# Kernel optimization log

Measured on AMD Instinct MI355X. Metric: run time of the kernel, lower is better.

Reference implementation:

```python
import jax, jax.numpy as jnp
import numpy as np

NUM_HEADS = 8


def setup_inputs() -> dict:
    key = jax.random.key(0)
    ks = jax.random.split(key, 7)
    B, D, N = 16, 512, 2048
    sc = 1.0 / np.sqrt(D)
    return {
        "X_Query": jax.random.normal(ks[0], (B, D, N), jnp.float32),
        "X_Key": jax.random.normal(ks[1], (B, D, N), jnp.float32),
        "X_Value": jax.random.normal(ks[2], (B, D, N), jnp.float32),
        "W_q": jax.random.normal(ks[3], (D, D), jnp.float32) * sc,
        "W_k": jax.random.normal(ks[4], (D, D), jnp.float32) * sc,
        "W_v": jax.random.normal(ks[5], (D, D), jnp.float32) * sc,
        "W_o": jax.random.normal(ks[6], (D, D), jnp.float32) * sc,
    }


def _proj(W, x):
    # Conv1d(D, D, kernel_size=1, bias=False) == channel matmul
    return jnp.einsum('oi,bin->bon', W, x)


def _split_heads(x, h):
    # torch: cat(x.chunk(h, dim=-1), dim=0) -> (h, B, D, N/h) stacked layout
    B, D, N = x.shape
    return x.reshape(B, D, h, N // h).transpose(2, 0, 1, 3)


def _mha(XQ, XK, XV, Wq, Wk, Wv, Wo):
    B, D, N = XQ.shape
    h = NUM_HEADS
    Nh = N // h
    q = _split_heads(_proj(Wq, XQ), h)  # (h, B, D, Nh)
    k = _split_heads(_proj(Wk, XK), h)
    v = _split_heads(_proj(Wv, XV), h)
    # scores over the CHANNEL axis: (h, B, D, D), scaled by sqrt(d_k)=sqrt(Nh)
    scores = jnp.einsum('hbdn,hben->hbde', q, k) / jnp.sqrt(jnp.asarray(Nh, q.dtype))
    p = jax.nn.softmax(scores, axis=-1)
    out = jnp.einsum('hbde,hben->hbdn', p, v)  # (h, B, D, Nh)
    # torch: cat(chunks, dim=0) inverse -> cat along dim=-1
    attn_heads = out.transpose(1, 2, 0, 3).reshape(B, D, N)
    return _proj(Wo, XQ - attn_heads)


def reference(X_Query, X_Key, X_Value, W_q, W_k, W_v, W_o):
    return _mha(X_Query, X_Key, X_Value, W_q, W_k, W_v, W_o)
```

## Files before the change

### kernel.cpp

```cpp
#include <hip/hip_runtime.h>
#include <hip/hip_bf16.h>

#define DD  512
#define NN  2048
#define BB  16
#define NHD 256

typedef unsigned short u16;
typedef __attribute__((ext_vector_type(4))) float f32x4;
typedef __attribute__((ext_vector_type(8))) short s16x8;
typedef __attribute__((ext_vector_type(4))) u16   u16x4;

static __device__ __forceinline__ u16 f2bf(float f) {
  __hip_bfloat16 h = __float2bfloat16(f);
  return *reinterpret_cast<u16*>(&h);
}
static __device__ __forceinline__ float bf2f(u16 u) {
  union { unsigned int i; float f; } v; v.i = ((unsigned int)u) << 16; return v.f;
}
static __device__ __forceinline__ f32x4 mfma_bf16(s16x8 a, s16x8 b, f32x4 c) {
  return __builtin_amdgcn_mfma_f32_16x16x32_bf16(a, b, c, 0, 0, 0);
}
static __device__ __forceinline__ void gload_lds16(const u16* g, u16* l) {
  __builtin_amdgcn_global_load_lds(
      (const __attribute__((address_space(1))) unsigned int*)g,
      (__attribute__((address_space(3))) unsigned int*)l, 16, 0, 0);
}
static __device__ __forceinline__ void barrier_raw() {
  __builtin_amdgcn_sched_barrier(0);
  __builtin_amdgcn_s_barrier();
  __builtin_amdgcn_sched_barrier(0);
}
#define WAITCNT(s) do { asm volatile("s_waitcnt " s ::: "memory"); \
                        __builtin_amdgcn_sched_barrier(0); } while (0)

__global__ __launch_bounds__(256) void k_cvt_w(const float* __restrict__ w0,
                                               const float* __restrict__ w1,
                                               const float* __restrict__ w2,
                                               const float* __restrict__ w3,
                                               u16* __restrict__ out) {
  const float* srcs[4] = {w0, w1, w2, w3};
  const float* s = srcs[blockIdx.y];
  u16* o = out + (size_t)blockIdx.y * (DD * DD);
  int idx = blockIdx.x * 256 + threadIdx.x;
  float4 v = *(const float4*)(s + (size_t)idx * 4);
  u16x4 u = {f2bf(v.x), f2bf(v.y), f2bf(v.z), f2bf(v.w)};
  *(u16x4*)(o + (size_t)idx * 4) = u;
}

__global__ __launch_bounds__(256) void k_transpose(const float* __restrict__ X,
                                                   u16* __restrict__ XT) {
  __shared__ float t[64][68];
  const int tid = threadIdx.x;
  const int n0 = blockIdx.x * 64, d0 = blockIdx.y * 64, b = blockIdx.z;
  const float* Xb = X + ((size_t)b * DD + d0) * NN + n0;
#pragma unroll
  for (int i = 0; i < 4; ++i) {
    int r = (tid >> 4) + i * 16;
    int c = (tid & 15) * 4;
    float4 v = *(const float4*)(Xb + (size_t)r * NN + c);
    t[r][c] = v.x; t[r][c + 1] = v.y; t[r][c + 2] = v.z; t[r][c + 3] = v.w;
  }
  __syncthreads();
  u16* Ob = XT + ((size_t)b * NN + n0) * DD + d0;
#pragma unroll
  for (int i = 0; i < 4; ++i) {
    int n = (tid >> 4) + i * 16;
    int d = (tid & 15) * 4;
    u16x4 u = {f2bf(t[d][n]), f2bf(t[d + 1][n]), f2bf(t[d + 2][n]), f2bf(t[d + 3][n])};
    *(u16x4*)(Ob + (size_t)n * DD + d) = u;
  }
}

#define GEMM_STAGE(Ag, lda, Bg, ldb, buf, kt)                                   \
  {                                                                             \
    _Pragma("unroll")                                                           \
    for (int j = 0; j < 4; ++j) {                                               \
      int s = j * 256 + w * 64 + lane;                                          \
      int row = s >> 3, u = s & 7;                                              \
      int col = ((u ^ (row & 7)) * 8);                                          \
      gload_lds16(Ag + (size_t)row * lda + (kt) * 64 + col, &Ab[buf][s * 8]);   \
      gload_lds16(Bg + (size_t)row * ldb + (kt) * 64 + col, &Bb[buf][s * 8]);   \
    }                                                                           \
  }

#define GEMM_COMPUTE(buf)                                                       \
  {                                                                             \
    _Pragma("unroll")                                                           \
    for (int ks = 0; ks < 2; ++ks) {                                            \
      s16x8 av[4], bv[4];                                                       \
      _Pragma("unroll")                                                         \
      for (int m = 0; m < 4; ++m) {                                             \
        int row = wm + m * 16 + r;                                              \
        av[m] = *(const s16x8*)&Ab[buf][row * 64 + (((ks * 4 + g) ^ (row & 7)) * 8)]; \
      }                                                                         \
      _Pragma("unroll")                                                         \
      for (int nf = 0; nf < 4; ++nf) {                                          \
        int row = wn + nf * 16 + r;                                             \
        bv[nf] = *(const s16x8*)&Bb[buf][row * 64 + (((ks * 4 + g) ^ (row & 7)) * 8)]; \
      }                                                                         \
      _Pragma("unroll")                                                         \
      for (int m = 0; m < 4; ++m)                                               \
        _Pragma("unroll")                                                       \
        for (int nf = 0; nf < 4; ++nf)                                          \
          acc[m][nf] = mfma_bf16(av[m], bv[nf], acc[m][nf]);                    \
    }                                                                           \
  }

#define GEMM_PREAMBLE                                                           \
  __shared__ __align__(16) u16 Ab[2][128 * 64];                                 \
  __shared__ __align__(16) u16 Bb[2][128 * 64];                                 \
  const int tid = threadIdx.x;                                                  \
  const int lane = tid & 63, w = tid >> 6;                                      \
  const int wm = (w >> 1) * 64, wn = (w & 1) * 64;                              \
  const int r = lane & 15, g = lane >> 4;                                       \
  f32x4 acc[4][4] = {};

#define GEMM_MAINLOOP(Ag, lda, Bg, ldb, nkt)                                    \
  GEMM_STAGE(Ag, lda, Bg, ldb, 0, 0);                                           \
  __syncthreads();                                                              \
  for (int kt = 0; kt < (nkt) - 1; ++kt) {                                      \
    GEMM_STAGE(Ag, lda, Bg, ldb, (kt & 1) ^ 1, kt + 1);                         \
    GEMM_COMPUTE(kt & 1);                                                       \
    __syncthreads();                                                            \
  }                                                                             \
  GEMM_COMPUTE(((nkt) - 1) & 1);

template <typename OUT_T>
__global__ __launch_bounds__(256) void k_gemm_nt(
    const u16* __restrict__ A, long long a_bs, int lda,
    const u16* __restrict__ B, long long b_bs, int ldb,
    OUT_T* __restrict__ C, long long c_bs, int ldc, int K) {
  GEMM_PREAMBLE
  const int m0 = blockIdx.x * 128, n0 = blockIdx.y * 128;
  const u16* Ag = A + (size_t)blockIdx.z * a_bs + (size_t)m0 * lda;
  const u16* Bg = B + (size_t)blockIdx.z * b_bs + (size_t)n0 * ldb;
  const int nkt = K >> 6;
  GEMM_MAINLOOP(Ag, lda, Bg, ldb, nkt);

  OUT_T* Cg = C + (size_t)blockIdx.z * c_bs;
#pragma unroll
  for (int m = 0; m < 4; ++m)
#pragma unroll
    for (int nf = 0; nf < 4; ++nf)
#pragma unroll
      for (int j = 0; j < 4; ++j) {
        int row = m0 + wm + m * 16 + g * 4 + j;
        int col = n0 + wn + nf * 16 + r;
        float v = acc[m][nf][j];
        if constexpr (sizeof(OUT_T) == 2) Cg[(size_t)row * ldc + col] = f2bf(v);
        else                              Cg[(size_t)row * ldc + col] = v;
      }
}

__global__ __launch_bounds__(512, 4) void k_attn_fused(
    const u16* __restrict__ Qdn, const u16* __restrict__ Kdn,
    const u16* __restrict__ VT,  const u16* __restrict__ XqT,
    u16* __restrict__ And) {
  __shared__ __align__(16) u16 L[37376];
  u16* Ks = L;
  u16* Vs = L + 16384;
  u16* Ps = L + 32768;

  const int tid = threadIdx.x;
  const int lane = tid & 63, w = tid >> 6;
  const int r = lane & 15, g = lane >> 4;
  const int dq = w >> 1, eh = w & 1;
  const int nq = w >> 1, dh = w & 1;
  const int bid = blockIdx.x;
  const int dt = bid >> 7, hb = bid & 127;
  const int h = hb & 7, b = hb >> 3;
  const int d0 = dt * 64, hn0 = h * NHD;

  const u16* Qg = Qdn + ((size_t)b * DD + d0) * NN + hn0;
  const u16* Kg = Kdn + ((size_t)b * DD) * NN + hn0;
  const u16* Vg = VT + ((size_t)b * NN + hn0) * DD;

  auto stage_k = [&](int idx) {
    const int e0 = (idx >> 1) * 64, c0 = (idx & 1) * 128;
    u16* dst = Ks + (idx & 1) * 8192;
#pragma unroll
    for (int j = 0; j < 2; ++j) {
      int s = j * 512 + tid;
      int row = s >> 4, u = s & 15;
      gload_lds16(Kg + (size_t)(e0 + row) * NN + c0 + ((u ^ (row & 7)) * 8), dst + s * 8);
    }
  };
  auto stage_v = [&](int t) {
    u16* dst = Vs + (t & 1) * 8192;
#pragma unroll
    for (int j = 0; j < 2; ++j) {
      int s = j * 512 + tid;
      int row = s >> 2, u = s & 3;
      gload_lds16(Vg + (size_t)row * DD + t * 32 + ((u ^ ((row >> 1) & 3)) * 8), dst + s * 8);
    }
  };

  stage_k(0);
#pragma unroll
  for (int j = 0; j < 4; ++j) {
    int s = j * 512 + tid;
    int row = s >> 5, u = s & 31;
    gload_lds16(Qg + (size_t)row * NN + ((u ^ (row & 7)) * 8), Vs + s * 8);
  }
  WAITCNT("vmcnt(0)");
  barrier_raw();
  s16x8 qf[8];
#pragma unroll
  for (int k2 = 0; k2 < 8; ++k2) {
    int row = dq * 16 + r;
    qf[k2] = *(const s16x8*)&Vs[row * 256 + (((k2 * 4 + g) ^ (row & 7)) * 8)];
  }
  WAITCNT("lgkmcnt(0)");
  barrier_raw();

  float psum[4] = {};
  f32x4 acc_o[4][2] = {};

  for (int et = 0; et < 8; ++et) {
    f32x4 acc_s[2] = {};
#pragma unroll
    for (int nsub = 0; nsub < 2; ++nsub) {
      const int idx = et * 2 + nsub;
      stage_v(idx);
      if (idx < 15) {
        stage_k(idx + 1);
        WAITCNT("vmcnt(4)");
      } else {
        WAITCNT("vmcnt(2)");
      }
      barrier_raw();
      const u16* kb = Ks + (idx & 1) * 8192;
#pragma unroll
      for (int kq = 0; kq < 4; ++kq) {
        s16x8 bv[2];
#pragma unroll
        for (int nf = 0; nf < 2; ++nf) {
          int rowe = eh * 32 + nf * 16 + r;
          bv[nf] = *(const s16x8*)&kb[rowe * 128 + (((kq * 4 + g) ^ (rowe & 7)) * 8)];
        }
        acc_s[0] = mfma_bf16(qf[nsub * 4 + kq], bv[0], acc_s[0]);
        acc_s[1] = mfma_bf16(qf[nsub * 4 + kq], bv[1], acc_s[1]);
      }
      WAITCNT("lgkmcnt(0)");
      barrier_raw();
    }
#pragma unroll
    for (int nf = 0; nf < 2; ++nf)
#pragma unroll
      for (int j = 0; j < 4; ++j) {
        int rowd = dq * 16 + g * 4 + j;
        int cole = eh * 32 + nf * 16 + r;
        float p = __expf(acc_s[nf][j] * 0.0625f);
        psum[j] += p;
        Ps[rowd * 72 + cole] = f2bf(p);
      }
    WAITCNT("lgkmcnt(0)");
    if (et < 7) WAITCNT("vmcnt(2)");
    else        WAITCNT("vmcnt(0)");
    barrier_raw();
#pragma unroll
    for (int vs = 0; vs < 2; ++vs) {
      s16x8 pb[2];
#pragma unroll
      for (int nf = 0; nf < 2; ++nf) {
        int rowd = dh * 32 + nf * 16 + r;
        pb[nf] = *(const s16x8*)&Ps[rowd * 72 + vs * 32 + g * 8];
      }
      const u16* vb = Vs + vs * 8192;
#pragma unroll
      for (int ms = 0; ms < 4; ++ms) {
        int rown = nq * 64 + ms * 16 + r;
        s16x8 av = *(const s16x8*)&vb[rown * 32 + ((g ^ ((rown >> 1) & 3)) * 8)];
        acc_o[ms][0] = mfma_bf16(av, pb[0], acc_o[ms][0]);
        acc_o[ms][1] = mfma_bf16(av, pb[1], acc_o[ms][1]);
      }
    }
    WAITCNT("lgkmcnt(0)");
    barrier_raw();
  }

  float* rs = (float*)L;
#pragma unroll
  for (int j = 0; j < 4; ++j) {
    float v = psum[j];
    v += __shfl_xor(v, 1);
    v += __shfl_xor(v, 2);
    v += __shfl_xor(v, 4);
    v += __shfl_xor(v, 8);
    if (r == 0) rs[w * 16 + g * 4 + j] = v;
  }
  __syncthreads();
  if (tid < 64) {
    int dqi = tid >> 4, i = tid & 15;
    rs[128 + tid] = 1.0f / (rs[(dqi * 2) * 16 + i] + rs[(dqi * 2 + 1) * 16 + i]);
  }
  __syncthreads();

  const u16* Xg = XqT + ((size_t)b * NN + hn0) * DD + d0;
  u16* Ag = And + ((size_t)b * NN + hn0) * DD + d0;
#pragma unroll
  for (int ms = 0; ms < 4; ++ms)
#pragma unroll
    for (int nf = 0; nf < 2; ++nf) {
      const int cold = dh * 32 + nf * 16 + r;
      const float inv = rs[128 + cold];
#pragma unroll
      for (int j = 0; j < 4; ++j) {
        const int npos = nq * 64 + ms * 16 + g * 4 + j;
        float o = acc_o[ms][nf][j] * inv;
        float xq = bf2f(Xg[(size_t)npos * DD + cold]);
        Ag[(size_t)npos * DD + cold] = f2bf(xq - o);
      }
    }
}

extern "C" void kernel_launch(void* const* d_in, const int* in_sizes, int n_in,
                              void* d_out, int out_size, void* d_ws, size_t ws_size,
                              hipStream_t stream) {
  const float* Xq = (const float*)d_in[0];
  const float* Xk = (const float*)d_in[1];
  const float* Xv = (const float*)d_in[2];
  const float* Wq = (const float*)d_in[3];
  const float* Wk = (const float*)d_in[4];
  const float* Wv = (const float*)d_in[5];
  const float* Wo = (const float*)d_in[6];
  float* out = (float*)d_out;

  char* ws = (char*)d_ws;
  const size_t MB = 1024 * 1024;
  u16* Wb  = (u16*)ws;
  u16* XqT = (u16*)(ws + 2 * MB);
  u16* Z2  = (u16*)(ws + 34 * MB);
  u16* And = Z2;
  u16* Qdn = (u16*)(ws + 66 * MB);
  u16* VTb = (u16*)d_out;
  u16* Kdn = (u16*)d_out + (size_t)BB * NN * DD;

  k_cvt_w<<<dim3(256, 4), 256, 0, stream>>>(Wq, Wk, Wv, Wo, Wb);

  k_transpose<<<dim3(NN / 64, DD / 64, BB), 256, 0, stream>>>(Xv, Z2);
  k_gemm_nt<u16><<<dim3(NN / 128, DD / 128, BB), 256, 0, stream>>>(
      Z2, (long long)NN * DD, DD,
      Wb + 2 * DD * DD, 0, DD,
      VTb, (long long)NN * DD, DD, DD);

  k_transpose<<<dim3(NN / 64, DD / 64, BB), 256, 0, stream>>>(Xq, XqT);
  k_gemm_nt<u16><<<dim3(DD / 128, NN / 128, BB), 256, 0, stream>>>(
      Wb, 0, DD,
      XqT, (long long)NN * DD, DD,
      Qdn, (long long)DD * NN, NN, DD);

  k_transpose<<<dim3(NN / 64, DD / 64, BB), 256, 0, stream>>>(Xk, Z2);
  k_gemm_nt<u16><<<dim3(DD / 128, NN / 128, BB), 256, 0, stream>>>(
      Wb + 1 * DD * DD, 0, DD,
      Z2, (long long)NN * DD, DD,
      Kdn, (long long)DD * NN, NN, DD);

  k_attn_fused<<<dim3(1024), 512, 0, stream>>>(Qdn, Kdn, VTb, XqT, And);

  k_gemm_nt<float><<<dim3(DD / 128, NN / 128, BB), 256, 0, stream>>>(
      Wb + 3 * DD * DD, 0, DD,
      And, (long long)NN * DD, DD,
      out, (long long)DD * NN, NN, DD);
}
```

Baseline: 254.2 us.

## Restructure fused attention into finer 3-stage K/V ring pipeline with smaller LDS

```diff
diff --git a/kernel.cpp b/kernel.cpp
--- a/kernel.cpp
+++ b/kernel.cpp
@@ -153,14 +153,14 @@
       }
 }
 
-__global__ __launch_bounds__(512, 4) void k_attn_fused(
+__global__ __launch_bounds__(512, 6) void k_attn_fused(
     const u16* __restrict__ Qdn, const u16* __restrict__ Kdn,
     const u16* __restrict__ VT,  const u16* __restrict__ XqT,
     u16* __restrict__ And) {
-  __shared__ __align__(16) u16 L[37376];
-  u16* Ks = L;
-  u16* Vs = L + 16384;
-  u16* Ps = L + 32768;
+  __shared__ __align__(16) u16 L[26624];
+  u16* Kr = L;
+  u16* Vr = L + 12288;
+  char* Psb = (char*)(L + 24576);
 
   const int tid = threadIdx.x;
   const int lane = tid & 63, w = tid >> 6;
@@ -176,105 +176,94 @@
   const u16* Kg = Kdn + ((size_t)b * DD) * NN + hn0;
   const u16* Vg = VT + ((size_t)b * NN + hn0) * DD;
 
-  auto stage_k = [&](int idx) {
-    const int e0 = (idx >> 1) * 64, c0 = (idx & 1) * 128;
-    u16* dst = Ks + (idx & 1) * 8192;
-#pragma unroll
-    for (int j = 0; j < 2; ++j) {
-      int s = j * 512 + tid;
-      int row = s >> 4, u = s & 15;
-      gload_lds16(Kg + (size_t)(e0 + row) * NN + c0 + ((u ^ (row & 7)) * 8), dst + s * 8);
-    }
+  auto stage_k = [&](int s) {
+    const int e0 = (s >> 1) * 32, n0 = (s & 1) * 128;
+    u16* dst = Kr + (s % 3) * 4096;
+    int row = tid >> 4, u = tid & 15;
+    gload_lds16(Kg + (size_t)(e0 + row) * NN + n0 + ((u ^ (row & 7)) * 8), dst + tid * 8);
   };
   auto stage_v = [&](int t) {
-    u16* dst = Vs + (t & 1) * 8192;
-#pragma unroll
-    for (int j = 0; j < 2; ++j) {
-      int s = j * 512 + tid;
-      int row = s >> 2, u = s & 3;
-      gload_lds16(Vg + (size_t)row * DD + t * 32 + ((u ^ ((row >> 1) & 3)) * 8), dst + s * 8);
-    }
+    const int e0 = (t >> 1) * 32, j = t & 1;
+    u16* dst = Vr + (t % 3) * 4096;
+    int rl = tid >> 2, u = tid & 3;
+    int gn = (rl >> 5) * 64 + j * 32 + (rl & 31);
+    gload_lds16(Vg + (size_t)gn * DD + e0 + ((u ^ (rl & 3)) * 8), dst + tid * 8);
   };
 
-  stage_k(0);
-#pragma unroll
-  for (int j = 0; j < 4; ++j) {
-    int s = j * 512 + tid;
+#pragma unroll
+  for (int jj = 0; jj < 4; ++jj) {
+    int s = jj * 512 + tid;
     int row = s >> 5, u = s & 31;
-    gload_lds16(Qg + (size_t)row * NN + ((u ^ (row & 7)) * 8), Vs + s * 8);
+    gload_lds16(Qg + (size_t)row * NN + ((u ^ (row & 7)) * 8), L + s * 8);
   }
   WAITCNT("vmcnt(0)");
   barrier_raw();
   s16x8 qf[8];
-#pragma unroll
-  for (int k2 = 0; k2 < 8; ++k2) {
-    int row = dq * 16 + r;
-    qf[k2] = *(const s16x8*)&Vs[row * 256 + (((k2 * 4 + g) ^ (row & 7)) * 8)];
+  {
+    const int qrow = dq * 16 + r;
+#pragma unroll
+    for (int k2 = 0; k2 < 8; ++k2)
+      qf[k2] = *(const s16x8*)&L[qrow * 256 + (((k2 * 4 + g) ^ (qrow & 7)) * 8)];
   }
   WAITCNT("lgkmcnt(0)");
   barrier_raw();
+  stage_k(0); stage_v(0); stage_k(1);
 
   float psum[4] = {};
-  f32x4 acc_o[4][2] = {};
-
-  for (int et = 0; et < 8; ++et) {
-    f32x4 acc_s[2] = {};
-#pragma unroll
-    for (int nsub = 0; nsub < 2; ++nsub) {
-      const int idx = et * 2 + nsub;
-      stage_v(idx);
-      if (idx < 15) {
-        stage_k(idx + 1);
-        WAITCNT("vmcnt(4)");
-      } else {
-        WAITCNT("vmcnt(2)");
-      }
+  f32x4 acc_o[2][2][2] = {};
+
+  for (int et = 0; et < 16; ++et) {
+    f32x4 acc_s = {};
+#pragma unroll
+    for (int cn = 0; cn < 2; ++cn) {
+      const int s = et * 2 + cn;
+      if (cn == 0)      WAITCNT("vmcnt(2)");
+      else if (et < 15) WAITCNT("vmcnt(2)");
+      else              WAITCNT("vmcnt(1)");
       barrier_raw();
-      const u16* kb = Ks + (idx & 1) * 8192;
+      if (s + 1 < 32) stage_v(s + 1);
+      if (s + 2 < 32) stage_k(s + 2);
+      const u16* kb = Kr + (s % 3) * 4096;
+      const int rowe = eh * 16 + r;
+      __builtin_amdgcn_s_setprio(1);
 #pragma unroll
       for (int kq = 0; kq < 4; ++kq) {
-        s16x8 bv[2];
-#pragma unroll
-        for (int nf = 0; nf < 2; ++nf) {
-          int rowe = eh * 32 + nf * 16 + r;
-          bv[nf] = *(const s16x8*)&kb[rowe * 128 + (((kq * 4 + g) ^ (rowe & 7)) * 8)];
-        }
-        acc_s[0] = mfma_bf16(qf[nsub * 4 + kq], bv[0], acc_s[0]);
-        acc_s[1] = mfma_bf16(qf[nsub * 4 + kq], bv[1], acc_s[1]);
-      }
+        s16x8 bv = *(const s16x8*)&kb[rowe * 128 + (((kq * 4 + g) ^ (rowe & 7)) * 8)];
+        acc_s = mfma_bf16(qf[cn * 4 + kq], bv, acc_s);
+      }
+      __builtin_amdgcn_s_setprio(0);
       WAITCNT("lgkmcnt(0)");
-      barrier_raw();
     }
 #pragma unroll
-    for (int nf = 0; nf < 2; ++nf)
-#pragma unroll
-      for (int j = 0; j < 4; ++j) {
-        int rowd = dq * 16 + g * 4 + j;
-        int cole = eh * 32 + nf * 16 + r;
-        float p = __expf(acc_s[nf][j] * 0.0625f);
-        psum[j] += p;
-        Ps[rowd * 72 + cole] = f2bf(p);
-      }
+    for (int j = 0; j < 4; ++j) {
+      int rowd = dq * 16 + g * 4 + j;
+      int cole = eh * 16 + r;
+      float p = __expf(acc_s[j] * 0.0625f);
+      psum[j] += p;
+      *(u16*)(Psb + rowd * 64 + (((cole * 2) ^ ((rowd & 3) << 4)))) = f2bf(p);
+    }
     WAITCNT("lgkmcnt(0)");
-    if (et < 7) WAITCNT("vmcnt(2)");
-    else        WAITCNT("vmcnt(0)");
+    if (et < 15) WAITCNT("vmcnt(3)");
+    else         WAITCNT("vmcnt(0)");
     barrier_raw();
 #pragma unroll
-    for (int vs = 0; vs < 2; ++vs) {
+    for (int j = 0; j < 2; ++j) {
+      const u16* vb = Vr + ((et * 2 + j) % 3) * 4096;
       s16x8 pb[2];
 #pragma unroll
       for (int nf = 0; nf < 2; ++nf) {
         int rowd = dh * 32 + nf * 16 + r;
-        pb[nf] = *(const s16x8*)&Ps[rowd * 72 + vs * 32 + g * 8];
-      }
-      const u16* vb = Vs + vs * 8192;
-#pragma unroll
-      for (int ms = 0; ms < 4; ++ms) {
-        int rown = nq * 64 + ms * 16 + r;
-        s16x8 av = *(const s16x8*)&vb[rown * 32 + ((g ^ ((rown >> 1) & 3)) * 8)];
-        acc_o[ms][0] = mfma_bf16(av, pb[0], acc_o[ms][0]);
-        acc_o[ms][1] = mfma_bf16(av, pb[1], acc_o[ms][1]);
-      }
+        pb[nf] = *(const s16x8*)(Psb + rowd * 64 + ((g * 16) ^ ((rowd & 3) << 4)));
+      }
+      __builtin_amdgcn_s_setprio(1);
+#pragma unroll
+      for (int ms = 0; ms < 2; ++ms) {
+        int rl = nq * 32 + ms * 16 + r;
+        s16x8 av = *(const s16x8*)((const char*)vb + rl * 64 + ((g * 16) ^ ((rl & 3) << 4)));
+        acc_o[j][ms][0] = mfma_bf16(av, pb[0], acc_o[j][ms][0]);
+        acc_o[j][ms][1] = mfma_bf16(av, pb[1], acc_o[j][ms][1]);
+      }
+      __builtin_amdgcn_s_setprio(0);
     }
     WAITCNT("lgkmcnt(0)");
     barrier_raw();
@@ -300,19 +289,21 @@
   const u16* Xg = XqT + ((size_t)b * NN + hn0) * DD + d0;
   u16* Ag = And + ((size_t)b * NN + hn0) * DD + d0;
 #pragma unroll
-  for (int ms = 0; ms < 4; ++ms)
-#pragma unroll
-    for (int nf = 0; nf < 2; ++nf) {
-      const int cold = dh * 32 + nf * 16 + r;
-      const float inv = rs[128 + cold];
-#pragma unroll
-      for (int j = 0; j < 4; ++j) {
-        const int npos = nq * 64 + ms * 16 + g * 4 + j;
-        float o = acc_o[ms][nf][j] * inv;
-        float xq = bf2f(Xg[(size_t)npos * DD + cold]);
-        Ag[(size_t)npos * DD + cold] = f2bf(xq - o);
-      }
-    }
+  for (int j = 0; j < 2; ++j)
+#pragma unroll
+    for (int ms = 0; ms < 2; ++ms)
+#pragma unroll
+      for (int nf = 0; nf < 2; ++nf) {
+        const int dc = dh * 32 + nf * 16 + r;
+        const float inv = rs[128 + dc];
+#pragma unroll
+        for (int jj = 0; jj < 4; ++jj) {
+          const int npos = nq * 64 + j * 32 + ms * 16 + g * 4 + jj;
+          float o = acc_o[j][ms][nf][jj] * inv;
+          float xq = bf2f(Xg[(size_t)npos * DD + dc]);
+          Ag[(size_t)npos * DD + dc] = f2bf(xq - o);
+        }
+      }
 }
 
 extern "C" void kernel_launch(void* const* d_in, const int* in_sizes, int n_in,
```

Measured after the change: 453.3 us. +78.3%, slower.
